# Kernel optimization log

Hardware: AMD Instinct MI355X
Metric: run time of the kernel (lower is better)

## Reference

```python
import jax, jax.numpy as jnp
import numpy as np


def _affinity(X, Y, W, b, gw):
    # torch Linear: W @ gw + b with W [out, in]
    coeff = jnp.tanh(W @ gw + b)              # [d]
    aff = (X * coeff) @ Y.T                   # [nx, ny]
    return jax.nn.softplus(aff) - 0.5


def _incidence(edge_index, num_nodes):
    # G[h, i] = 1, H[t, i] = 1 -- scatter instead of python loop
    e = edge_index.shape[1]
    cols = jnp.arange(e)
    G = jnp.zeros((num_nodes, e), jnp.float32).at[edge_index[0], cols].set(1.0)
    H = jnp.zeros((num_nodes, e), jnp.float32).at[edge_index[1], cols].set(1.0)
    return G, H


def setup_inputs() -> dict:
    key = jax.random.key(0)
    ks = jax.random.split(key, 9)
    n1 = n2 = 48
    e1 = e2 = 192
    gd = dn = de = 1024
    return {
        "x1": jax.random.normal(ks[0], (n1, dn), jnp.float32),
        "x2": jax.random.normal(ks[1], (n2, dn), jnp.float32),
        "ef1": jax.random.normal(ks[2], (e1, de), jnp.float32),
        "ef2": jax.random.normal(ks[3], (e2, de), jnp.float32),
        "global_weight": jax.random.normal(ks[4], (gd,), jnp.float32),
        "Wn": jax.random.normal(ks[5], (dn, gd), jnp.float32) / np.sqrt(gd).astype(np.float32),
        "bn": jnp.zeros((dn,), jnp.float32),
        "We": jax.random.normal(ks[6], (de, gd), jnp.float32) / np.sqrt(gd).astype(np.float32),
        "be": jnp.zeros((de,), jnp.float32),
        "edge_index1": jax.random.randint(ks[7], (2, e1), 0, n1, dtype=jnp.int32),
        "edge_index2": jax.random.randint(ks[8], (2, e2), 0, n2, dtype=jnp.int32),
    }


def reference(x1, x2, ef1, ef2, global_weight, Wn, bn, We, be, edge_index1, edge_index2):
    n1, n2 = x1.shape[0], x2.shape[0]
    Mp = jax.nn.relu(_affinity(x1, x2, Wn, bn, global_weight))    # [n1, n2]
    Me = jax.nn.relu(_affinity(ef1, ef2, We, be, global_weight))  # [e1, e2]
    G1, H1 = _incidence(edge_index1, n1)
    G2, H2 = _incidence(edge_index2, n2)
    Kg = jnp.kron(G2, G1)  # [n2*n1, e2*e1]
    Kh = jnp.kron(H2, H1)  # [n2*n1, e2*e1]
    vec_Mp = Mp.reshape(-1)  # [n1*n2]
    vec_Me = Me.reshape(-1)  # [e1*e2]
    # diag(vec_Me) @ Kh.T == row-scaled Kh.T; diag(vec_Mp) added on the diagonal.
    # Same math as the torch eye/diag construction, without materializing eye.
    M = jnp.diag(vec_Mp) + Kg @ (vec_Me[:, None] * Kh.T)  # [n1*n2, n1*n2]
    return M
```

## Files before the change

kernel.cpp:

```cpp
#include <hip/hip_runtime.h>
#include <math.h>

#define D     1024
#define N1    48
#define E1    192
#define NOUT  2304
#define NE    36864
#define KS    8

__global__ void coeff_kernel(const float* __restrict__ Wn, const float* __restrict__ bn,
                             const float* __restrict__ We, const float* __restrict__ be,
                             const float* __restrict__ gw, float* __restrict__ coeff) {
    int row = blockIdx.x;
    const float* W; const float* b; int d;
    if (row < D) { W = Wn; b = bn; d = row; }
    else         { W = We; b = be; d = row - D; }
    int t = threadIdx.x;
    float4 w = *(const float4*)(W + (size_t)d * D + t * 4);
    float4 g = *(const float4*)(gw + t * 4);
    float s = w.x * g.x + w.y * g.y + w.z * g.z + w.w * g.w;
    #pragma unroll
    for (int off = 32; off > 0; off >>= 1) s += __shfl_down(s, off);
    __shared__ float red[4];
    if ((t & 63) == 0) red[t >> 6] = s;
    __syncthreads();
    if (t == 0) {
        float tot = red[0] + red[1] + red[2] + red[3];
        coeff[row] = tanhf(tot + b[d]);
    }
}

__global__ void affinity_partial_kernel(const float* __restrict__ x1, const float* __restrict__ x2,
                                        const float* __restrict__ ef1, const float* __restrict__ ef2,
                                        const float* __restrict__ coeff,
                                        float* __restrict__ Mp_part, float* __restrict__ Me_part) {
    __shared__ float As[16][68];
    __shared__ float Bs[16][68];
    int bid = blockIdx.x;
    const float *A, *B, *cf; float* out; int ncols, tiles_x, tile, ks;
    if (bid < 9 * KS) {
        tile = bid >> 3; ks = bid & 7;
        A = x1; B = x2; cf = coeff; out = Mp_part + ks * NOUT; ncols = N1; tiles_x = 3;
    } else {
        int b = bid - 9 * KS;
        tile = b >> 3; ks = b & 7;
        A = ef1; B = ef2; cf = coeff + D; out = Me_part + ks * NE; ncols = E1; tiles_x = 12;
    }
    int ty = tile / tiles_x, tx = tile - ty * tiles_x;

    int t  = threadIdx.x;
    int r  = t >> 4;
    int cb = (t & 15) << 2;
    int cc = t & 15;
    size_t rowA = (size_t)(ty * 16 + r);
    size_t rowB = (size_t)(tx * 16 + r);
    float acc = 0.f;
    #pragma unroll
    for (int ch = 0; ch < 2; ch++) {
        int k0 = ks * 128 + ch * 64;
        float4 a = *(const float4*)(A + rowA * D + k0 + cb);
        float4 c = *(const float4*)(cf + k0 + cb);
        float4 b = *(const float4*)(B + rowB * D + k0 + cb);
        *(float4*)&As[r][cb] = make_float4(a.x * c.x, a.y * c.y, a.z * c.z, a.w * c.w);
        *(float4*)&Bs[r][cb] = b;
        __syncthreads();
        #pragma unroll
        for (int kk = 0; kk < 64; kk += 4) {
            float4 av = *(const float4*)&As[r][kk];
            float4 bv = *(const float4*)&Bs[cc][kk];
            acc = fmaf(av.x, bv.x, acc);
            acc = fmaf(av.y, bv.y, acc);
            acc = fmaf(av.z, bv.z, acc);
            acc = fmaf(av.w, bv.w, acc);
        }
        __syncthreads();
    }
    out[(size_t)(ty * 16 + r) * ncols + tx * 16 + cc] = acc;
}

__device__ __forceinline__ float act(float x) {
    float sp = fmaxf(x, 0.f) + log1pf(expf(-fabsf(x)));
    return fmaxf(sp - 0.5f, 0.f);
}

__global__ void init_out_kernel(float* __restrict__ M, const float* __restrict__ Mp_part) {
    int idx = blockIdx.x * blockDim.x + threadIdx.x;
    if (idx >= NOUT * (NOUT / 4)) return;
    int r = idx / (NOUT / 4);
    int c = (idx - r * (NOUT / 4)) << 2;
    float4 v = make_float4(0.f, 0.f, 0.f, 0.f);
    int d = r - c;
    if (d >= 0 && d < 4) {
        float s = 0.f;
        #pragma unroll
        for (int ks = 0; ks < KS; ks++) s += Mp_part[ks * NOUT + r];
        ((float*)&v)[d] = act(s);
    }
    *(float4*)(M + (size_t)r * NOUT + c) = v;
}

__global__ void scatter_kernel(float* __restrict__ M, const float* __restrict__ Me_part,
                               const int* __restrict__ ei1, const int* __restrict__ ei2) {
    int q = blockIdx.x * blockDim.x + threadIdx.x;
    if (q >= NE) return;
    float s = 0.f;
    #pragma unroll
    for (int ks = 0; ks < KS; ks++) s += Me_part[ks * NE + q];
    float v = act(s);
    if (v > 0.f) {
        int b2 = q / E1;
        int b1 = q - b2 * E1;
        int r = ei2[b2]      * N1 + ei1[b1];
        int c = ei2[E1 + b2] * N1 + ei1[E1 + b1];
        atomicAdd(M + (size_t)r * NOUT + c, v);
    }
}

extern "C" void kernel_launch(void* const* d_in, const int* in_sizes, int n_in,
                              void* d_out, int out_size, void* d_ws, size_t ws_size,
                              hipStream_t stream) {
    const float* x1  = (const float*)d_in[0];
    const float* x2  = (const float*)d_in[1];
    const float* ef1 = (const float*)d_in[2];
    const float* ef2 = (const float*)d_in[3];
    const float* gw  = (const float*)d_in[4];
    const float* Wn  = (const float*)d_in[5];
    const float* bn  = (const float*)d_in[6];
    const float* We  = (const float*)d_in[7];
    const float* be  = (const float*)d_in[8];
    const int*   ei1 = (const int*)d_in[9];
    const int*   ei2 = (const int*)d_in[10];

    float* M  = (float*)d_out;
    float* ws = (float*)d_ws;
    float* coeff   = ws;
    float* Mp_part = ws + 2048;
    float* Me_part = Mp_part + KS * NOUT;

    coeff_kernel<<<2 * D, 256, 0, stream>>>(Wn, bn, We, be, gw, coeff);
    affinity_partial_kernel<<<(9 + 144) * KS, 256, 0, stream>>>(x1, x2, ef1, ef2, coeff,
                                                                Mp_part, Me_part);
    init_out_kernel<<<(NOUT * (NOUT / 4) + 255) / 256, 256, 0, stream>>>(M, Mp_part);
    scatter_kernel<<<(NE + 255) / 256, 256, 0, stream>>>(M, Me_part, ei1, ei2);
}
```

Before: 112.7 us.

## Fuse output zeroing into affinity kernel and merge diagonal with scatter

The 21 MB output zero-fill now runs as extra blocks inside the affinity GEMM launch, so the memset overlaps the small GEMM and one launch is removed. The diagonal Mp write moves into the scatter kernel as atomic adds on top of the zeroed buffer, which merges the former init and scatter launches into one. The zero-fill blocks use wider per-thread stores of four float4 each. The risk is that the diagonal now uses atomics.

```diff
diff --git a/kernel.cpp b/kernel.cpp
--- a/kernel.cpp
+++ b/kernel.cpp
@@ -7,6 +7,11 @@
 #define NOUT  2304
 #define NE    36864
 #define KS    8
+
+#define AFF_BLOCKS  ((9 + 144) * KS)
+#define ZERO_BLOCKS (NOUT * NOUT / 4096)
+#define SCAT_BLOCKS (NE / 256)
+#define DIAG_BLOCKS (NOUT / 256)
 
 __global__ void coeff_kernel(const float* __restrict__ Wn, const float* __restrict__ bn,
                              const float* __restrict__ We, const float* __restrict__ be,
@@ -30,13 +35,25 @@
     }
 }
 
-__global__ void affinity_partial_kernel(const float* __restrict__ x1, const float* __restrict__ x2,
-                                        const float* __restrict__ ef1, const float* __restrict__ ef2,
-                                        const float* __restrict__ coeff,
-                                        float* __restrict__ Mp_part, float* __restrict__ Me_part) {
+__global__ void affinity_zero_kernel(const float* __restrict__ x1, const float* __restrict__ x2,
+                                     const float* __restrict__ ef1, const float* __restrict__ ef2,
+                                     const float* __restrict__ coeff,
+                                     float* __restrict__ Mp_part, float* __restrict__ Me_part,
+                                     float* __restrict__ M) {
     __shared__ float As[16][68];
     __shared__ float Bs[16][68];
     int bid = blockIdx.x;
+    int t = threadIdx.x;
+
+    if (bid >= AFF_BLOCKS) {
+        size_t base = (size_t)(bid - AFF_BLOCKS) * 4096 + t * 4;
+        float4 z = make_float4(0.f, 0.f, 0.f, 0.f);
+        #pragma unroll
+        for (int p = 0; p < 4; p++)
+            *(float4*)(M + base + p * 1024) = z;
+        return;
+    }
+
     const float *A, *B, *cf; float* out; int ncols, tiles_x, tile, ks;
     if (bid < 9 * KS) {
         tile = bid >> 3; ks = bid & 7;
@@ -48,7 +65,6 @@
     }
     int ty = tile / tiles_x, tx = tile - ty * tiles_x;
 
-    int t  = threadIdx.x;
     int r  = t >> 4;
     int cb = (t & 15) << 2;
     int cc = t & 15;
@@ -83,36 +99,32 @@
     return fmaxf(sp - 0.5f, 0.f);
 }
 
-__global__ void init_out_kernel(float* __restrict__ M, const float* __restrict__ Mp_part) {
-    int idx = blockIdx.x * blockDim.x + threadIdx.x;
-    if (idx >= NOUT * (NOUT / 4)) return;
-    int r = idx / (NOUT / 4);
-    int c = (idx - r * (NOUT / 4)) << 2;
-    float4 v = make_float4(0.f, 0.f, 0.f, 0.f);
-    int d = r - c;
-    if (d >= 0 && d < 4) {
+__global__ void scatter_diag_kernel(float* __restrict__ M,
+                                    const float* __restrict__ Mp_part,
+                                    const float* __restrict__ Me_part,
+                                    const int* __restrict__ ei1, const int* __restrict__ ei2) {
+    int bid = blockIdx.x;
+    int t = threadIdx.x;
+    if (bid < SCAT_BLOCKS) {
+        int q = bid * 256 + t;
+        float s = 0.f;
+        #pragma unroll
+        for (int ks = 0; ks < KS; ks++) s += Me_part[ks * NE + q];
+        float v = act(s);
+        if (v > 0.f) {
+            int b2 = q / E1;
+            int b1 = q - b2 * E1;
+            int r = ei2[b2]      * N1 + ei1[b1];
+            int c = ei2[E1 + b2] * N1 + ei1[E1 + b1];
+            atomicAdd(M + (size_t)r * NOUT + c, v);
+        }
+    } else {
+        int r = (bid - SCAT_BLOCKS) * 256 + t;
         float s = 0.f;
         #pragma unroll
         for (int ks = 0; ks < KS; ks++) s += Mp_part[ks * NOUT + r];
-        ((float*)&v)[d] = act(s);
-    }
-    *(float4*)(M + (size_t)r * NOUT + c) = v;
-}
-
-__global__ void scatter_kernel(float* __restrict__ M, const float* __restrict__ Me_part,
-                               const int* __restrict__ ei1, const int* __restrict__ ei2) {
-    int q = blockIdx.x * blockDim.x + threadIdx.x;
-    if (q >= NE) return;
-    float s = 0.f;
-    #pragma unroll
-    for (int ks = 0; ks < KS; ks++) s += Me_part[ks * NE + q];
-    float v = act(s);
-    if (v > 0.f) {
-        int b2 = q / E1;
-        int b1 = q - b2 * E1;
-        int r = ei2[b2]      * N1 + ei1[b1];
-        int c = ei2[E1 + b2] * N1 + ei1[E1 + b1];
-        atomicAdd(M + (size_t)r * NOUT + c, v);
+        float v = act(s);
+        if (v > 0.f) atomicAdd(M + (size_t)r * NOUT + r, v);
     }
 }
 
@@ -138,8 +150,8 @@
     float* Me_part = Mp_part + KS * NOUT;
 
     coeff_kernel<<<2 * D, 256, 0, stream>>>(Wn, bn, We, be, gw, coeff);
-    affinity_partial_kernel<<<(9 + 144) * KS, 256, 0, stream>>>(x1, x2, ef1, ef2, coeff,
-                                                                Mp_part, Me_part);
-    init_out_kernel<<<(NOUT * (NOUT / 4) + 255) / 256, 256, 0, stream>>>(M, Mp_part);
-    scatter_kernel<<<(NE + 255) / 256, 256, 0, stream>>>(M, Me_part, ei1, ei2);
+    affinity_zero_kernel<<<AFF_BLOCKS + ZERO_BLOCKS, 256, 0, stream>>>(
+        x1, x2, ef1, ef2, coeff, Mp_part, Me_part, M);
+    scatter_diag_kernel<<<SCAT_BLOCKS + DIAG_BLOCKS, 256, 0, stream>>>(
+        M, Mp_part, Me_part, ei1, ei2);
 }
```

Result: faster. 94.42 us (-16.2%).

## Fuse split-K reduction and scatter via last-block atomics; zero output in prep kernel

Applied to the files above, without the earlier changes.

The coefficient computation and the zeroing of the output matrix and workspace accumulators now run in one prep kernel. The affinity kernel accumulates its split-K partials with atomics into a single buffer. A per-tile counter picks the last-arriving block, which applies the activation and scatters the result into M, either onto the diagonal or at the edge-pair position. This cuts four launches to two and drops the separate partial-sum reads and the diagonal-aware init pass. In exchange it adds atomic traffic, fences and counter contention, and float atomics make the summation order nondeterministic.

```diff
diff --git a/kernel.cpp b/kernel.cpp
--- a/kernel.cpp
+++ b/kernel.cpp
@@ -8,47 +8,78 @@
 #define NE    36864
 #define KS    8
 
-__global__ void coeff_kernel(const float* __restrict__ Wn, const float* __restrict__ bn,
-                             const float* __restrict__ We, const float* __restrict__ be,
-                             const float* __restrict__ gw, float* __restrict__ coeff) {
-    int row = blockIdx.x;
-    const float* W; const float* b; int d;
-    if (row < D) { W = Wn; b = bn; d = row; }
-    else         { W = We; b = be; d = row - D; }
+#define MP_TILES 9
+#define ME_TILES 144
+
+#define COEFF_ITEMS  (2 * D)
+#define MZERO_ITEMS  (NOUT * NOUT / 4096)
+#define WSZERO_ITEMS 10
+#define K1_GRID      (COEFF_ITEMS + MZERO_ITEMS + WSZERO_ITEMS)
+
+#define K2_GRID      ((MP_TILES + ME_TILES) * KS)
+
+__device__ __forceinline__ float act(float x) {
+    float sp = fmaxf(x, 0.f) + log1pf(expf(-fabsf(x)));
+    return fmaxf(sp - 0.5f, 0.f);
+}
+
+__global__ void prep_kernel(const float* __restrict__ Wn, const float* __restrict__ bn,
+                            const float* __restrict__ We, const float* __restrict__ be,
+                            const float* __restrict__ gw, float* __restrict__ coeff,
+                            float* __restrict__ M, float* __restrict__ zacc) {
+    int bid = blockIdx.x;
     int t = threadIdx.x;
-    float4 w = *(const float4*)(W + (size_t)d * D + t * 4);
-    float4 g = *(const float4*)(gw + t * 4);
-    float s = w.x * g.x + w.y * g.y + w.z * g.z + w.w * g.w;
-    #pragma unroll
-    for (int off = 32; off > 0; off >>= 1) s += __shfl_down(s, off);
-    __shared__ float red[4];
-    if ((t & 63) == 0) red[t >> 6] = s;
-    __syncthreads();
-    if (t == 0) {
-        float tot = red[0] + red[1] + red[2] + red[3];
-        coeff[row] = tanhf(tot + b[d]);
+    if (bid < COEFF_ITEMS) {
+        const float* W; const float* b; int d;
+        if (bid < D) { W = Wn; b = bn; d = bid; }
+        else         { W = We; b = be; d = bid - D; }
+        float4 w = *(const float4*)(W + (size_t)d * D + t * 4);
+        float4 g = *(const float4*)(gw + t * 4);
+        float s = w.x * g.x + w.y * g.y + w.z * g.z + w.w * g.w;
+        #pragma unroll
+        for (int off = 32; off > 0; off >>= 1) s += __shfl_down(s, off);
+        __shared__ float red[4];
+        if ((t & 63) == 0) red[t >> 6] = s;
+        __syncthreads();
+        if (t == 0) coeff[bid] = tanhf(red[0] + red[1] + red[2] + red[3] + b[d]);
+    } else if (bid < COEFF_ITEMS + MZERO_ITEMS) {
+        size_t base = (size_t)(bid - COEFF_ITEMS) * 4096 + t * 4;
+        float4 z = make_float4(0.f, 0.f, 0.f, 0.f);
+        #pragma unroll
+        for (int p = 0; p < 4; p++) *(float4*)(M + base + p * 1024) = z;
+    } else {
+        size_t base = (size_t)(bid - COEFF_ITEMS - MZERO_ITEMS) * 4096 + t * 4;
+        float4 z = make_float4(0.f, 0.f, 0.f, 0.f);
+        #pragma unroll
+        for (int p = 0; p < 4; p++) *(float4*)(zacc + base + p * 1024) = z;
     }
 }
 
-__global__ void affinity_partial_kernel(const float* __restrict__ x1, const float* __restrict__ x2,
-                                        const float* __restrict__ ef1, const float* __restrict__ ef2,
-                                        const float* __restrict__ coeff,
-                                        float* __restrict__ Mp_part, float* __restrict__ Me_part) {
+__global__ __launch_bounds__(256)
+void affinity_scatter_kernel(const float* __restrict__ x1, const float* __restrict__ x2,
+                             const float* __restrict__ ef1, const float* __restrict__ ef2,
+                             const float* __restrict__ coeff,
+                             const int* __restrict__ ei1, const int* __restrict__ ei2,
+                             float* __restrict__ Mp_acc, float* __restrict__ Me_acc,
+                             int* __restrict__ cnt, float* __restrict__ M) {
     __shared__ float As[16][68];
     __shared__ float Bs[16][68];
+    __shared__ int isLast;
     int bid = blockIdx.x;
-    const float *A, *B, *cf; float* out; int ncols, tiles_x, tile, ks;
-    if (bid < 9 * KS) {
+    int t = threadIdx.x;
+
+    const float *A, *B, *cf; float* accbuf; int tile, ks, ncols, tiles_x, cntIdx; bool isMp;
+    if (bid < MP_TILES * KS) {
         tile = bid >> 3; ks = bid & 7;
-        A = x1; B = x2; cf = coeff; out = Mp_part + ks * NOUT; ncols = N1; tiles_x = 3;
+        A = x1; B = x2; cf = coeff; accbuf = Mp_acc;
+        ncols = N1; tiles_x = 3; cntIdx = tile; isMp = true;
     } else {
-        int b = bid - 9 * KS;
+        int b = bid - MP_TILES * KS;
         tile = b >> 3; ks = b & 7;
-        A = ef1; B = ef2; cf = coeff + D; out = Me_part + ks * NE; ncols = E1; tiles_x = 12;
+        A = ef1; B = ef2; cf = coeff + D; accbuf = Me_acc;
+        ncols = E1; tiles_x = 12; cntIdx = MP_TILES + tile; isMp = false;
     }
     int ty = tile / tiles_x, tx = tile - ty * tiles_x;
-
-    int t  = threadIdx.x;
     int r  = t >> 4;
     int cb = (t & 15) << 2;
     int cc = t & 15;
@@ -75,44 +106,26 @@
         }
         __syncthreads();
     }
-    out[(size_t)(ty * 16 + r) * ncols + tx * 16 + cc] = acc;
-}
 
-__device__ __forceinline__ float act(float x) {
-    float sp = fmaxf(x, 0.f) + log1pf(expf(-fabsf(x)));
-    return fmaxf(sp - 0.5f, 0.f);
-}
+    int elem = (ty * 16 + r) * ncols + tx * 16 + cc;
+    atomicAdd(&accbuf[elem], acc);
+    __threadfence();
+    __syncthreads();
+    if (t == 0) isLast = (atomicAdd(&cnt[cntIdx], 1) == KS - 1);
+    __syncthreads();
+    if (!isLast) return;
 
-__global__ void init_out_kernel(float* __restrict__ M, const float* __restrict__ Mp_part) {
-    int idx = blockIdx.x * blockDim.x + threadIdx.x;
-    if (idx >= NOUT * (NOUT / 4)) return;
-    int r = idx / (NOUT / 4);
-    int c = (idx - r * (NOUT / 4)) << 2;
-    float4 v = make_float4(0.f, 0.f, 0.f, 0.f);
-    int d = r - c;
-    if (d >= 0 && d < 4) {
-        float s = 0.f;
-        #pragma unroll
-        for (int ks = 0; ks < KS; ks++) s += Mp_part[ks * NOUT + r];
-        ((float*)&v)[d] = act(s);
-    }
-    *(float4*)(M + (size_t)r * NOUT + c) = v;
-}
-
-__global__ void scatter_kernel(float* __restrict__ M, const float* __restrict__ Me_part,
-                               const int* __restrict__ ei1, const int* __restrict__ ei2) {
-    int q = blockIdx.x * blockDim.x + threadIdx.x;
-    if (q >= NE) return;
-    float s = 0.f;
-    #pragma unroll
-    for (int ks = 0; ks < KS; ks++) s += Me_part[ks * NE + q];
+    float s = __hip_atomic_load(&accbuf[elem], __ATOMIC_RELAXED, __HIP_MEMORY_SCOPE_AGENT);
     float v = act(s);
     if (v > 0.f) {
-        int b2 = q / E1;
-        int b1 = q - b2 * E1;
-        int r = ei2[b2]      * N1 + ei1[b1];
-        int c = ei2[E1 + b2] * N1 + ei1[E1 + b1];
-        atomicAdd(M + (size_t)r * NOUT + c, v);
+        if (isMp) {
+            atomicAdd(M + (size_t)elem * NOUT + elem, v);
+        } else {
+            int b2 = ty * 16 + r, b1 = tx * 16 + cc;
+            int rr  = ei2[b2]      * N1 + ei1[b1];
+            int ccc = ei2[E1 + b2] * N1 + ei1[E1 + b1];
+            atomicAdd(M + (size_t)rr * NOUT + ccc, v);
+        }
     }
 }
 
@@ -133,13 +146,12 @@
 
     float* M  = (float*)d_out;
     float* ws = (float*)d_ws;
-    float* coeff   = ws;
-    float* Mp_part = ws + 2048;
-    float* Me_part = Mp_part + KS * NOUT;
+    float* coeff  = ws;
+    float* Mp_acc = ws + 2048;
+    float* Me_acc = Mp_acc + NOUT;
+    int*   cnt    = (int*)(Me_acc + NE);
 
-    coeff_kernel<<<2 * D, 256, 0, stream>>>(Wn, bn, We, be, gw, coeff);
-    affinity_partial_kernel<<<(9 + 144) * KS, 256, 0, stream>>>(x1, x2, ef1, ef2, coeff,
-                                                                Mp_part, Me_part);
-    init_out_kernel<<<(NOUT * (NOUT / 4) + 255) / 256, 256, 0, stream>>>(M, Mp_part);
-    scatter_kernel<<<(NE + 255) / 256, 256, 0, stream>>>(M, Me_part, ei1, ei2);
+    prep_kernel<<<K1_GRID, 256, 0, stream>>>(Wn, bn, We, be, gw, coeff, M, Mp_acc);
+    affinity_scatter_kernel<<<K2_GRID, 256, 0, stream>>>(
+        x1, x2, ef1, ef2, coeff, ei1, ei2, Mp_acc, Me_acc, cnt, M);
 }
```

Result: slower. 164.5 us (+46.0%).
